# Performance work log

Hardware: AMD Instinct MI355X
Metric: run time of the kernel (lower is better)

Reference implementation:

```python
import jax, jax.numpy as jnp
import numpy as np
from jax import lax

K = 7            # pool_size / PSROI_BINS
C_OUT = 10       # output channels per bin (features has K*K*C_OUT channels)
FEAT_STRIDE = 16
LAMDA = 0.1
SAMPLES = 2      # bilinear sample points per bin side
H = W = 200
C_IN = K * K * C_OUT  # 490
N_ROIS = 512


def setup_inputs() -> dict:
    key = jax.random.key(0)
    k1, k2, k3, k4 = jax.random.split(key, 4)
    features = jax.random.normal(k1, (1, H, W, C_IN), jnp.float32)
    conv_w = jax.random.truncated_normal(k2, -2.0, 2.0, (3, 3, C_IN, 2 * K * K), jnp.float32) * 0.01
    img = H * FEAT_STRIDE  # image-space extent
    cxy = jax.random.uniform(k3, (N_ROIS, 2), minval=0.0, maxval=img - 1.0)
    wh = jax.random.uniform(k4, (N_ROIS, 2), minval=64.0, maxval=640.0)
    x1 = jnp.clip(cxy[:, 0] - wh[:, 0] * 0.5, 0.0, img - 2.0)
    y1 = jnp.clip(cxy[:, 1] - wh[:, 1] * 0.5, 0.0, img - 2.0)
    x2 = jnp.clip(x1 + wh[:, 0], x1 + 1.0, img - 1.0)
    y2 = jnp.clip(y1 + wh[:, 1], y1 + 1.0, img - 1.0)
    rois = jnp.stack([jnp.zeros(N_ROIS), x1, y1, x2, y2], axis=-1)  # [N,5]
    return {"features": features, "rois": rois, "conv_w": conv_w}


def _bilinear(feat, y, x):
    """feat [H,W,C]; y,x arbitrary equal shapes -> [..., C]."""
    Hf, Wf = feat.shape[0], feat.shape[1]
    y = jnp.clip(y, 0.0, Hf - 1.0)
    x = jnp.clip(x, 0.0, Wf - 1.0)
    y0 = jnp.floor(y)
    x0 = jnp.floor(x)
    y0i = y0.astype(jnp.int32)
    x0i = x0.astype(jnp.int32)
    y1i = jnp.minimum(y0i + 1, Hf - 1)
    x1i = jnp.minimum(x0i + 1, Wf - 1)
    wy = (y - y0)[..., None]
    wx = (x - x0)[..., None]
    v00 = feat[y0i, x0i]
    v01 = feat[y0i, x1i]
    v10 = feat[y1i, x0i]
    v11 = feat[y1i, x1i]
    return (v00 * (1 - wy) * (1 - wx) + v01 * (1 - wy) * wx
            + v10 * wy * (1 - wx) + v11 * wy * wx)


def _ps_roi(feat, box, cpg, offsets):
    """Position-sensitive RoI avg pooling with optional per-bin offsets.
    feat [H,W,K*K*cpg]; box (x1,y1,x2,y2) image coords; offsets [K,K,2] (dx,dy)
    in image coords or None. Returns [K,K,cpg]."""
    x1, y1, x2, y2 = box
    fx1 = x1 / FEAT_STRIDE
    fy1 = y1 / FEAT_STRIDE
    bw = (x2 - x1 + 1.0) / FEAT_STRIDE / K
    bh = (y2 - y1 + 1.0) / FEAT_STRIDE / K
    idx = jnp.arange(K, dtype=feat.dtype)
    s = (jnp.arange(SAMPLES, dtype=feat.dtype) + 0.5) / SAMPLES
    sx = fx1 + (idx[:, None] + s[None, :]) * bw  # [K(j), S]
    sy = fy1 + (idx[:, None] + s[None, :]) * bh  # [K(i), S]
    gx = jnp.broadcast_to(sx[None, :, None, :], (K, K, SAMPLES, SAMPLES))
    gy = jnp.broadcast_to(sy[:, None, :, None], (K, K, SAMPLES, SAMPLES))
    if offsets is not None:
        off = offsets / FEAT_STRIDE  # image -> feature coords
        gx = gx + off[..., 0][:, :, None, None]
        gy = gy + off[..., 1][:, :, None, None]
    vals = _bilinear(feat, gy, gx)                     # [K,K,S,S,K*K*cpg]
    vals = vals.reshape(K, K, SAMPLES, SAMPLES, K * K, cpg)
    bin_idx = (jnp.arange(K)[:, None] * K + jnp.arange(K)[None, :])  # [K,K]
    sel = jnp.take_along_axis(
        vals, bin_idx[:, :, None, None, None, None], axis=4)[..., 0, :]
    return sel.mean(axis=(2, 3))  # [K,K,cpg]


def reference(features, rois, conv_w):
    # 3x3 same conv producing 2*K*K offset channels (no bias)
    offset_map = lax.conv_general_dilated(
        features, conv_w, (1, 1), 'SAME',
        dimension_numbers=('NHWC', 'HWIO', 'NHWC'))[0]  # [H,W,2*K*K]
    feat0 = features[0]  # [H,W,K*K*C_OUT]

    def one_roi(roi):
        x1, y1, x2, y2 = roi[1], roi[2], roi[3], roi[4]
        rw = x2 - x1 + 1.0
        rh = y2 - y1 + 1.0
        box = (x1, y1, x2, y2)
        # stage 1: pool the offset map position-sensitively -> [K,K,2]
        off = _ps_roi(offset_map, box, 2, None).reshape(-1, 2)
        off = jnp.stack((off[:, 0] * rw * LAMDA,
                         off[:, 1] * rh * LAMDA), axis=-1).reshape(K, K, 2)
        # stage 2: deformable PS-RoI pooling of the features -> [K,K,C_OUT]
        return _ps_roi(feat0, box, C_OUT, off)

    return jax.vmap(one_roi)(rois)  # [N, K, K, C_OUT]
```

## Files before the change

### kernel.cpp

```cpp
#include <hip/hip_runtime.h>
#include <hip/hip_bf16.h>

#define Hh   200
#define Ww   200
#define CIN  490
#define OCN  98
#define KK   7
#define COUT 10
#define NROIS 512
#define PIX  8

#define PH   202
#define PW   202
#define PC   512
#define NPIX (Hh * Ww)
#define KCN  16
#define NF   7
#define NUNITS 144
#define NGRAN  36
#define MR   2
#define NWAVES 5
#define BLK_M (NWAVES * MR * 16)

typedef __attribute__((ext_vector_type(8))) short short8;
typedef __attribute__((ext_vector_type(4))) float float4v;

__global__ __launch_bounds__(256) void pack_feat_kernel(
    const float* __restrict__ feat, __hip_bfloat16* __restrict__ pf)
{
    int tid = blockIdx.x * 256 + threadIdx.x;
    if (tid >= PH * PW * (PC / 8)) return;
    int c8  = (tid & 63) * 8;
    int pix = tid >> 6;
    int py = pix / PW, px = pix % PW;
    __hip_bfloat16* dst = pf + (size_t)pix * PC + c8;
    bool interior = (py >= 1 && py <= Hh && px >= 1 && px <= Ww);

    __hip_bfloat16 v[8];
    if (interior && c8 + 8 <= CIN) {
        const float* s = feat + ((size_t)(py - 1) * Ww + (px - 1)) * CIN + c8;
#pragma unroll
        for (int q = 0; q < 4; ++q) {
            float2 f2 = *reinterpret_cast<const float2*>(s + q * 2);
            v[q * 2]     = __float2bfloat16(f2.x);
            v[q * 2 + 1] = __float2bfloat16(f2.y);
        }
    } else {
        const float* s = interior ? feat + ((size_t)(py - 1) * Ww + (px - 1)) * CIN : nullptr;
#pragma unroll
        for (int j = 0; j < 8; ++j) {
            float val = (interior && (c8 + j) < CIN) ? s[c8 + j] : 0.f;
            v[j] = __float2bfloat16(val);
        }
    }
    *reinterpret_cast<short8*>(dst) = *reinterpret_cast<short8*>(v);
}

__global__ __launch_bounds__(256) void pack_w_kernel(
    const float* __restrict__ w, __hip_bfloat16* __restrict__ bp)
{
    int idx = blockIdx.x * 256 + threadIdx.x;
    if (idx >= NUNITS * NF * 64 * 8) return;
    int j = idx & 7;
    int l = (idx >> 3) & 63;
    int f = (idx >> 9) % NF;
    int u = idx / (NF * 512);
    int tap = u / KCN, kc = u % KCN;
    int k = kc * 32 + ((l >> 4) * 8) + j;
    int n = f * 16 + (l & 15);
    float val = (k < CIN && n < OCN) ? w[((size_t)tap * CIN + k) * OCN + n] : 0.f;
    bp[idx] = __float2bfloat16(val);
}

__global__ __launch_bounds__(320) void conv_mfma_kernel(
    const short* __restrict__ pf,
    const short* __restrict__ bp,
    float* __restrict__ om)
{
    __shared__ short bsm[8 * 3584];

    int orig = blockIdx.x;
    int xcd = orig & 7;
    int pos = orig >> 3;
    int blk = ((xcd < 2) ? xcd * 32 : 64 + (xcd - 2) * 31) + pos;

    int l = threadIdx.x & 63;
    int w = threadIdx.x >> 6;
    int m0 = blk * BLK_M + w * (MR * 16);

    const short* abase0;
    const short* abase1;
    {
        int row0 = m0 + (l & 15);
        int row1 = m0 + 16 + (l & 15);
        int y0 = row0 / Ww, x0 = row0 % Ww;
        int y1 = row1 / Ww, x1 = row1 % Ww;
        abase0 = pf + ((size_t)(y0 * PW + x0) * PC) + ((l >> 4) * 8);
        abase1 = pf + ((size_t)(y1 * PW + x1) * PC) + ((l >> 4) * 8);
    }
    const short* bbase = bp + l * 8;

    float4v acc[MR][NF];
#pragma unroll
    for (int r = 0; r < MR; ++r)
#pragma unroll
        for (int f = 0; f < NF; ++f) acc[r][f] = (float4v){0.f, 0.f, 0.f, 0.f};

    auto aOff = [&](int u) -> int {
        int tap = u >> 4, kc = u & 15;
        int ky = tap / 3, kx = tap % 3;
        return (ky * PW + kx) * PC + kc * 32;
    };

#pragma unroll
    for (int s = 0; s < 6; ++s) {
        int i = w + s * NWAVES;
        if (i < 28) {
            int u = i / 7, f = i % 7;
            short8 v = *reinterpret_cast<const short8*>(
                bp + ((size_t)(u * NF + f)) * 512 + l * 8);
            *reinterpret_cast<short8*>(&bsm[(u & 7) * 3584 + f * 512 + l * 8]) = v;
        }
    }
    short8 a00 = *reinterpret_cast<const short8*>(abase0 + aOff(0));
    short8 a01 = *reinterpret_cast<const short8*>(abase0 + aOff(1));
    short8 a02 = *reinterpret_cast<const short8*>(abase0 + aOff(2));
    short8 a03 = *reinterpret_cast<const short8*>(abase0 + aOff(3));
    short8 a10 = *reinterpret_cast<const short8*>(abase1 + aOff(0));
    short8 a11 = *reinterpret_cast<const short8*>(abase1 + aOff(1));
    short8 a12 = *reinterpret_cast<const short8*>(abase1 + aOff(2));
    short8 a13 = *reinterpret_cast<const short8*>(abase1 + aOff(3));
    __syncthreads();

    for (int g = 0; g < NGRAN; ++g) {
        bool more = (g < NGRAN - 1);
        int u0n = (g + 1) * 4;

        short8 st0, st1, st2, st3, st4, st5;
        int off0 = -1, off1 = -1, off2 = -1, off3 = -1, off4 = -1, off5 = -1;
        if (more) {
#define STAGE_LOAD(S, STV, OFFV)                                               \
            {                                                                  \
                int i = w + (S) * NWAVES;                                      \
                if (i < 28) {                                                  \
                    int uu = u0n + i / 7, f = i % 7;                           \
                    STV = *reinterpret_cast<const short8*>(                    \
                        bp + ((size_t)(uu * NF + f)) * 512 + l * 8);           \
                    OFFV = (uu & 7) * 3584 + f * 512 + l * 8;                  \
                }                                                              \
            }
            STAGE_LOAD(0, st0, off0)
            STAGE_LOAD(1, st1, off1)
            STAGE_LOAD(2, st2, off2)
            STAGE_LOAD(3, st3, off3)
            STAGE_LOAD(4, st4, off4)
            STAGE_LOAD(5, st5, off5)
#undef STAGE_LOAD
        }
        short8 n00, n01, n02, n03, n10, n11, n12, n13;
        if (more) {
            n00 = *reinterpret_cast<const short8*>(abase0 + aOff(u0n + 0));
            n01 = *reinterpret_cast<const short8*>(abase0 + aOff(u0n + 1));
            n02 = *reinterpret_cast<const short8*>(abase0 + aOff(u0n + 2));
            n03 = *reinterpret_cast<const short8*>(abase0 + aOff(u0n + 3));
            n10 = *reinterpret_cast<const short8*>(abase1 + aOff(u0n + 0));
            n11 = *reinterpret_cast<const short8*>(abase1 + aOff(u0n + 1));
            n12 = *reinterpret_cast<const short8*>(abase1 + aOff(u0n + 2));
            n13 = *reinterpret_cast<const short8*>(abase1 + aOff(u0n + 3));
        }

        int u0 = g * 4;
#define COMPUTE_UNIT(J, AR0, AR1)                                               \
        {                                                                       \
            int sbase = ((u0 + J) & 7) * 3584 + l * 8;                          \
            _Pragma("unroll")                                                   \
            for (int f = 0; f < NF; ++f) {                                      \
                short8 b = *reinterpret_cast<short8*>(&bsm[sbase + f * 512]);   \
                acc[0][f] = __builtin_amdgcn_mfma_f32_16x16x32_bf16(            \
                    AR0, b, acc[0][f], 0, 0, 0);                                \
                acc[1][f] = __builtin_amdgcn_mfma_f32_16x16x32_bf16(            \
                    AR1, b, acc[1][f], 0, 0, 0);                                \
            }                                                                   \
        }
        COMPUTE_UNIT(0, a00, a10)
        COMPUTE_UNIT(1, a01, a11)
        COMPUTE_UNIT(2, a02, a12)
        COMPUTE_UNIT(3, a03, a13)
#undef COMPUTE_UNIT

        if (off0 >= 0) *reinterpret_cast<short8*>(&bsm[off0]) = st0;
        if (off1 >= 0) *reinterpret_cast<short8*>(&bsm[off1]) = st1;
        if (off2 >= 0) *reinterpret_cast<short8*>(&bsm[off2]) = st2;
        if (off3 >= 0) *reinterpret_cast<short8*>(&bsm[off3]) = st3;
        if (off4 >= 0) *reinterpret_cast<short8*>(&bsm[off4]) = st4;
        if (off5 >= 0) *reinterpret_cast<short8*>(&bsm[off5]) = st5;
        if (more) {
            a00 = n00; a01 = n01; a02 = n02; a03 = n03;
            a10 = n10; a11 = n11; a12 = n12; a13 = n13;
        }
        __syncthreads();
    }

    int n = l & 15;
#pragma unroll
    for (int r = 0; r < MR; ++r) {
        int rbase = m0 + r * 16 + ((l >> 4) * 4);
#pragma unroll
        for (int f = 0; f < NF; ++f) {
            int col = f * 16 + n;
            if (col < OCN) {
#pragma unroll
                for (int j = 0; j < 4; ++j)
                    om[(size_t)(rbase + j) * OCN + col] = acc[r][f][j];
            }
        }
    }
}

__global__ __launch_bounds__(256) void conv3x3_kernel(
    const float* __restrict__ feat, const float* __restrict__ w,
    const float* __restrict__ zero, float* __restrict__ om)
{
    int idx = blockIdx.x * blockDim.x + threadIdx.x;
    if (idx >= Hh * (Ww / PIX) * OCN) return;
    int oc = idx % OCN;
    int g  = idx / OCN;
    int x0 = (g % (Ww / PIX)) * PIX;
    int y  = g / (Ww / PIX);

    float acc[PIX];
#pragma unroll
    for (int p = 0; p < PIX; ++p) acc[p] = 0.f;

    for (int ky = 0; ky < 3; ++ky) {
        int yy = y + ky - 1;
        if (yy < 0 || yy >= Hh) continue;
        const float* frow = feat + (size_t)yy * Ww * CIN;
        for (int kx = 0; kx < 3; ++kx) {
            const float* wp = w + ((ky * 3 + kx) * CIN) * OCN + oc;
            const float* fp[PIX];
#pragma unroll
            for (int p = 0; p < PIX; ++p) {
                int xx = x0 + p + kx - 1;
                fp[p] = (xx >= 0 && xx < Ww) ? (frow + (size_t)xx * CIN) : zero;
            }
            for (int ic = 0; ic < CIN; ic += 2) {
                float w0 = wp[ic * OCN];
                float w1 = wp[(ic + 1) * OCN];
#pragma unroll
                for (int p = 0; p < PIX; ++p) {
                    float2 f = *reinterpret_cast<const float2*>(fp[p] + ic);
                    acc[p] = fmaf(f.x, w0, acc[p]);
                    acc[p] = fmaf(f.y, w1, acc[p]);
                }
            }
        }
    }
    float* orow = om + ((size_t)y * Ww + x0) * OCN + oc;
#pragma unroll
    for (int p = 0; p < PIX; ++p) orow[p * OCN] = acc[p];
}

__device__ __forceinline__ void bilin_setup(float y, float x,
    int& i00, int& i01, int& i10, int& i11,
    float& w00, float& w01, float& w10, float& w11)
{
    y = fminf(fmaxf(y, 0.f), 199.f);
    x = fminf(fmaxf(x, 0.f), 199.f);
    float y0f = floorf(y), x0f = floorf(x);
    int y0 = (int)y0f, x0i = (int)x0f;
    int y1 = min(y0 + 1, 199), x1 = min(x0i + 1, 199);
    float wy = y - y0f, wx = x - x0f;
    i00 = y0 * Ww + x0i;  i01 = y0 * Ww + x1;
    i10 = y1 * Ww + x0i;  i11 = y1 * Ww + x1;
    w00 = (1.f - wy) * (1.f - wx);
    w01 = (1.f - wy) * wx;
    w10 = wy * (1.f - wx);
    w11 = wy * wx;
}

__global__ __launch_bounds__(256) void psroi_kernel(
    const float* __restrict__ feat, const float* __restrict__ rois,
    const float* __restrict__ om, float* __restrict__ out)
{
    int n = blockIdx.x;
    int t = threadIdx.x;

    float x1 = rois[n * 5 + 1], y1 = rois[n * 5 + 2];
    float x2 = rois[n * 5 + 3], y2 = rois[n * 5 + 4];
    float rw = x2 - x1 + 1.0f, rh = y2 - y1 + 1.0f;
    float fx1 = x1 * 0.0625f, fy1 = y1 * 0.0625f;
    float bw = (rw * 0.0625f) / 7.0f;
    float bh = (rh * 0.0625f) / 7.0f;

    __shared__ float offs[49][2];

    if (t < 49) {
        int bi = t / 7, bj = t % 7;
        float ax = 0.f, ay = 0.f;
#pragma unroll
        for (int ss = 0; ss < 4; ++ss) {
            float sj = ((float)(ss & 1) + 0.5f) * 0.5f;
            float si = ((float)(ss >> 1) + 0.5f) * 0.5f;
            float gx = fx1 + ((float)bj + sj) * bw;
            float gy = fy1 + ((float)bi + si) * bh;
            int i00, i01, i10, i11; float w00, w01, w10, w11;
            bilin_setup(gy, gx, i00, i01, i10, i11, w00, w01, w10, w11);
            int c0 = t * 2;
            const float* p00 = om + (size_t)i00 * OCN + c0;
            const float* p01 = om + (size_t)i01 * OCN + c0;
            const float* p10 = om + (size_t)i10 * OCN + c0;
            const float* p11 = om + (size_t)i11 * OCN + c0;
            ax += w00 * p00[0] + w01 * p01[0] + w10 * p10[0] + w11 * p11[0];
            ay += w00 * p00[1] + w01 * p01[1] + w10 * p10[1] + w11 * p11[1];
        }
        offs[t][0] = ax * 0.25f * rw * 0.1f * 0.0625f;
        offs[t][1] = ay * 0.25f * rh * 0.1f * 0.0625f;
    }
    __syncthreads();

    for (int o = t; o < KK * KK * COUT; o += blockDim.x) {
        int bin = o / COUT, c = o % COUT;
        int bi = bin / 7, bj = bin % 7;
        float dx = offs[bin][0], dy = offs[bin][1];
        int ch = bin * COUT + c;
        float acc = 0.f;
#pragma unroll
        for (int ss = 0; ss < 4; ++ss) {
            float sj = ((float)(ss & 1) + 0.5f) * 0.5f;
            float si = ((float)(ss >> 1) + 0.5f) * 0.5f;
            float gx = fx1 + ((float)bj + sj) * bw + dx;
            float gy = fy1 + ((float)bi + si) * bh + dy;
            int i00, i01, i10, i11; float w00, w01, w10, w11;
            bilin_setup(gy, gx, i00, i01, i10, i11, w00, w01, w10, w11);
            acc += w00 * feat[(size_t)i00 * CIN + ch]
                 + w01 * feat[(size_t)i01 * CIN + ch]
                 + w10 * feat[(size_t)i10 * CIN + ch]
                 + w11 * feat[(size_t)i11 * CIN + ch];
        }
        out[(size_t)n * (KK * KK * COUT) + o] = acc * 0.25f;
    }
}

extern "C" void kernel_launch(void* const* d_in, const int* in_sizes, int n_in,
                              void* d_out, int out_size, void* d_ws, size_t ws_size,
                              hipStream_t stream) {
    const float* feat = (const float*)d_in[0];
    const float* rois = (const float*)d_in[1];
    const float* w    = (const float*)d_in[2];
    float* out = (float*)d_out;

    const size_t OM_BYTES = (size_t)NPIX * OCN * 4;
    const size_t BP_BYTES = (size_t)NUNITS * NF * 64 * 8 * 2;
    const size_t PF_BYTES = (size_t)PH * PW * PC * 2;
    const size_t NEEDED = OM_BYTES + BP_BYTES + PF_BYTES;

    if (ws_size >= NEEDED) {
        float* om = (float*)d_ws;
        __hip_bfloat16* bp = (__hip_bfloat16*)((char*)d_ws + OM_BYTES);
        __hip_bfloat16* pf = (__hip_bfloat16*)((char*)d_ws + OM_BYTES + BP_BYTES);

        int wThreads = NUNITS * NF * 64 * 8;
        pack_w_kernel<<<(wThreads + 255) / 256, 256, 0, stream>>>(w, bp);
        int fThreads = PH * PW * (PC / 8);
        pack_feat_kernel<<<(fThreads + 255) / 256, 256, 0, stream>>>(feat, pf);
        conv_mfma_kernel<<<250, 320, 0, stream>>>(
            (const short*)pf, (const short*)bp, om);
        psroi_kernel<<<NROIS, 256, 0, stream>>>(feat, rois, om, out);
    } else {
        float* zero = (float*)d_ws;
        float* om   = (float*)d_ws + 1024;
        hipMemsetAsync(d_ws, 0, 4096, stream);
        int convThreads = Hh * (Ww / PIX) * OCN;
        conv3x3_kernel<<<(convThreads + 255) / 256, 256, 0, stream>>>(feat, w, zero, om);
        psroi_kernel<<<NROIS, 256, 0, stream>>>(feat, rois, om, out);
    }
}
```

Measured before the change: 106.0 us.

## Split conv MFMA K-loop across two wave groups with LDS reduction

The conv MFMA kernel now launches 10 waves per block instead of 5. The two halves of the block each process half of the 144 K-units, using separate LDS weight buffers, and their partial accumulators are summed through LDS before the output is written. The weight packing order is changed to kc-major so each half's units are contiguous. The intent is to raise parallelism and latency hiding on 250 blocks that underfill the GPU, at the cost of doubled LDS, an extra reduction pass, and removal of the XCD-aware block remapping.

```diff
diff --git a/kernel.cpp b/kernel.cpp
--- a/kernel.cpp
+++ b/kernel.cpp
@@ -17,10 +17,8 @@
 #define KCN  16
 #define NF   7
 #define NUNITS 144
-#define NGRAN  36
-#define MR   2
-#define NWAVES 5
-#define BLK_M (NWAVES * MR * 16)
+#define HGRAN  18
+#define HALF_SHORTS (8 * 3584)
 
 typedef __attribute__((ext_vector_type(8))) short short8;
 typedef __attribute__((ext_vector_type(4))) float float4v;
@@ -65,28 +63,26 @@
     int l = (idx >> 3) & 63;
     int f = (idx >> 9) % NF;
     int u = idx / (NF * 512);
-    int tap = u / KCN, kc = u % KCN;
+    int kc = u / 9, tap = u % 9;
     int k = kc * 32 + ((l >> 4) * 8) + j;
     int n = f * 16 + (l & 15);
     float val = (k < CIN && n < OCN) ? w[((size_t)tap * CIN + k) * OCN + n] : 0.f;
     bp[idx] = __float2bfloat16(val);
 }
 
-__global__ __launch_bounds__(320) void conv_mfma_kernel(
+__global__ __launch_bounds__(640) void conv_mfma_kernel(
     const short* __restrict__ pf,
     const short* __restrict__ bp,
     float* __restrict__ om)
 {
-    __shared__ short bsm[8 * 3584];
-
-    int orig = blockIdx.x;
-    int xcd = orig & 7;
-    int pos = orig >> 3;
-    int blk = ((xcd < 2) ? xcd * 32 : 64 + (xcd - 2) * 31) + pos;
+    __shared__ short bsm[2 * HALF_SHORTS];
 
     int l = threadIdx.x & 63;
     int w = threadIdx.x >> 6;
-    int m0 = blk * BLK_M + w * (MR * 16);
+    int mpos = w % 5;
+    int ks = w / 5;
+    int ubase = ks * 72;
+    int m0 = blockIdx.x * 160 + mpos * 32;
 
     const short* abase0;
     const short* abase1;
@@ -98,55 +94,56 @@
         abase0 = pf + ((size_t)(y0 * PW + x0) * PC) + ((l >> 4) * 8);
         abase1 = pf + ((size_t)(y1 * PW + x1) * PC) + ((l >> 4) * 8);
     }
-    const short* bbase = bp + l * 8;
-
-    float4v acc[MR][NF];
-#pragma unroll
-    for (int r = 0; r < MR; ++r)
+
+    float4v acc[2][NF];
+#pragma unroll
+    for (int r = 0; r < 2; ++r)
 #pragma unroll
         for (int f = 0; f < NF; ++f) acc[r][f] = (float4v){0.f, 0.f, 0.f, 0.f};
 
     auto aOff = [&](int u) -> int {
-        int tap = u >> 4, kc = u & 15;
-        int ky = tap / 3, kx = tap % 3;
+        int kc = u / 9, tap = u - kc * 9;
+        int ky = tap / 3, kx = tap - ky * 3;
         return (ky * PW + kx) * PC + kc * 32;
     };
+    int lbase = ks * HALF_SHORTS;
 
 #pragma unroll
     for (int s = 0; s < 6; ++s) {
-        int i = w + s * NWAVES;
+        int i = mpos + s * 5;
         if (i < 28) {
-            int u = i / 7, f = i % 7;
+            int uu = ubase + i / 7, f = i % 7;
             short8 v = *reinterpret_cast<const short8*>(
-                bp + ((size_t)(u * NF + f)) * 512 + l * 8);
-            *reinterpret_cast<short8*>(&bsm[(u & 7) * 3584 + f * 512 + l * 8]) = v;
-        }
-    }
-    short8 a00 = *reinterpret_cast<const short8*>(abase0 + aOff(0));
-    short8 a01 = *reinterpret_cast<const short8*>(abase0 + aOff(1));
-    short8 a02 = *reinterpret_cast<const short8*>(abase0 + aOff(2));
-    short8 a03 = *reinterpret_cast<const short8*>(abase0 + aOff(3));
-    short8 a10 = *reinterpret_cast<const short8*>(abase1 + aOff(0));
-    short8 a11 = *reinterpret_cast<const short8*>(abase1 + aOff(1));
-    short8 a12 = *reinterpret_cast<const short8*>(abase1 + aOff(2));
-    short8 a13 = *reinterpret_cast<const short8*>(abase1 + aOff(3));
+                bp + ((size_t)(uu * NF + f)) * 512 + l * 8);
+            *reinterpret_cast<short8*>(
+                &bsm[lbase + (uu & 7) * 3584 + f * 512 + l * 8]) = v;
+        }
+    }
+    short8 a00 = *reinterpret_cast<const short8*>(abase0 + aOff(ubase + 0));
+    short8 a01 = *reinterpret_cast<const short8*>(abase0 + aOff(ubase + 1));
+    short8 a02 = *reinterpret_cast<const short8*>(abase0 + aOff(ubase + 2));
+    short8 a03 = *reinterpret_cast<const short8*>(abase0 + aOff(ubase + 3));
+    short8 a10 = *reinterpret_cast<const short8*>(abase1 + aOff(ubase + 0));
+    short8 a11 = *reinterpret_cast<const short8*>(abase1 + aOff(ubase + 1));
+    short8 a12 = *reinterpret_cast<const short8*>(abase1 + aOff(ubase + 2));
+    short8 a13 = *reinterpret_cast<const short8*>(abase1 + aOff(ubase + 3));
     __syncthreads();
 
-    for (int g = 0; g < NGRAN; ++g) {
-        bool more = (g < NGRAN - 1);
-        int u0n = (g + 1) * 4;
+    for (int g = 0; g < HGRAN; ++g) {
+        bool more = (g < HGRAN - 1);
+        int u0n = ubase + (g + 1) * 4;
 
         short8 st0, st1, st2, st3, st4, st5;
         int off0 = -1, off1 = -1, off2 = -1, off3 = -1, off4 = -1, off5 = -1;
         if (more) {
 #define STAGE_LOAD(S, STV, OFFV)                                               \
             {                                                                  \
-                int i = w + (S) * NWAVES;                                      \
+                int i = mpos + (S) * 5;                                        \
                 if (i < 28) {                                                  \
                     int uu = u0n + i / 7, f = i % 7;                           \
                     STV = *reinterpret_cast<const short8*>(                    \
                         bp + ((size_t)(uu * NF + f)) * 512 + l * 8);           \
-                    OFFV = (uu & 7) * 3584 + f * 512 + l * 8;                  \
+                    OFFV = lbase + (uu & 7) * 3584 + f * 512 + l * 8;          \
                 }                                                              \
             }
             STAGE_LOAD(0, st0, off0)
@@ -169,10 +166,10 @@
             n13 = *reinterpret_cast<const short8*>(abase1 + aOff(u0n + 3));
         }
 
-        int u0 = g * 4;
+        int u0 = ubase + g * 4;
 #define COMPUTE_UNIT(J, AR0, AR1)                                               \
         {                                                                       \
-            int sbase = ((u0 + J) & 7) * 3584 + l * 8;                          \
+            int sbase = lbase + ((u0 + J) & 7) * 3584 + l * 8;                  \
             _Pragma("unroll")                                                   \
             for (int f = 0; f < NF; ++f) {                                      \
                 short8 b = *reinterpret_cast<short8*>(&bsm[sbase + f * 512]);   \
@@ -201,17 +198,33 @@
         __syncthreads();
     }
 
-    int n = l & 15;
-#pragma unroll
-    for (int r = 0; r < MR; ++r) {
-        int rbase = m0 + r * 16 + ((l >> 4) * 4);
-#pragma unroll
-        for (int f = 0; f < NF; ++f) {
-            int col = f * 16 + n;
-            if (col < OCN) {
-#pragma unroll
-                for (int j = 0; j < 4; ++j)
-                    om[(size_t)(rbase + j) * OCN + col] = acc[r][f][j];
+    float* lred = (float*)bsm;
+    if (ks == 1) {
+#pragma unroll
+        for (int r = 0; r < 2; ++r)
+#pragma unroll
+            for (int f = 0; f < NF; ++f) {
+                int idx = (((mpos * 2 + r) * NF + f) * 64 + l) * 4;
+                *reinterpret_cast<float4v*>(&lred[idx]) = acc[r][f];
+            }
+    }
+    __syncthreads();
+    if (ks == 0) {
+        int n = l & 15;
+#pragma unroll
+        for (int r = 0; r < 2; ++r) {
+            int rbase = m0 + r * 16 + ((l >> 4) * 4);
+#pragma unroll
+            for (int f = 0; f < NF; ++f) {
+                int idx = (((mpos * 2 + r) * NF + f) * 64 + l) * 4;
+                float4v other = *reinterpret_cast<float4v*>(&lred[idx]);
+                float4v tot = acc[r][f] + other;
+                int col = f * 16 + n;
+                if (col < OCN) {
+#pragma unroll
+                    for (int j = 0; j < 4; ++j)
+                        om[(size_t)(rbase + j) * OCN + col] = tot[j];
+                }
             }
         }
     }
@@ -364,7 +377,7 @@
         pack_w_kernel<<<(wThreads + 255) / 256, 256, 0, stream>>>(w, bp);
         int fThreads = PH * PW * (PC / 8);
         pack_feat_kernel<<<(fThreads + 255) / 256, 256, 0, stream>>>(feat, pf);
-        conv_mfma_kernel<<<250, 320, 0, stream>>>(
+        conv_mfma_kernel<<<250, 640, 0, stream>>>(
             (const short*)pf, (const short*)bp, om);
         psroi_kernel<<<NROIS, 256, 0, stream>>>(feat, rois, om, out);
     } else {
```

After: 108.6 us. 1.02x slower.
